# Optimization experiments

Hardware: AMD Instinct MI355X
Metric: run time of the kernel (lower is better)

## Reference

```python
import jax, jax.numpy as jnp
import numpy as np

B, S, FEAT, DK = 128, 2048, 512, 64

def setup_inputs() -> dict:
    key = jax.random.key(0)
    k1, k2, k3, k4, k5 = jax.random.split(key, 5)
    input_k = jax.random.normal(k1, (B, S, FEAT), dtype=jnp.float32)
    input_q = jax.random.normal(k2, (B, FEAT), dtype=jnp.float32)
    context_len = jax.random.randint(k3, (B,), 0, S + 1, dtype=jnp.int32)
    # Linear weights stored as [in, out] so y = x @ W
    W_K = jax.random.normal(k4, (FEAT, DK), dtype=jnp.float32) / np.sqrt(FEAT)
    W_Q = jax.random.normal(k5, (FEAT, DK), dtype=jnp.float32) / np.sqrt(FEAT)
    return {"input_k": input_k, "input_q": input_q, "context_len": context_len,
            "W_K": W_K, "W_Q": W_Q}

def reference(input_k, input_q, context_len, W_K, W_Q):
    # K: [B,S,dk], q: [B,dk]
    K = jnp.einsum('bsf,fd->bsd', input_k, W_K)
    q = input_q @ W_Q
    scores = jnp.einsum('bd,bsd->bs', q, K)  # [B,S] (n_heads=1, no scaling in original)
    mask = jnp.arange(S)[None, :] < context_len[:, None]  # [B,S]
    attn = jax.nn.softmax(jnp.where(mask, scores, -1e30), axis=-1)  # [B,S]
    context = jnp.einsum('bs,bsf->bf', attn, input_k)  # [B,FEAT]
    # length==0 rows produce zeros in the original
    context = jnp.where((context_len > 0)[:, None], context, 0.0)
    return context
```

## Files before the change

### kernel.cpp

```cpp
#include <hip/hip_runtime.h>
#include <math.h>

#define B_    128
#define S_    2048
#define FEAT_ 512
#define DK_   64
#define NSPLIT 32
#define RSTRIDE (NSPLIT * FEAT_)

typedef float f32x4 __attribute__((ext_vector_type(4)));

__device__ __forceinline__ float dot8(f32x4 x0, f32x4 x1, f32x4 v0, f32x4 v1) {
  float p = x0[0] * v0[0];
  p = fmaf(x0[1], v0[1], p);
  p = fmaf(x0[2], v0[2], p);
  p = fmaf(x0[3], v0[3], p);
  p = fmaf(x1[0], v1[0], p);
  p = fmaf(x1[1], v1[1], p);
  p = fmaf(x1[2], v1[2], p);
  p = fmaf(x1[3], v1[3], p);
  return p;
}

__device__ __forceinline__ float wredsum(float p) {
#pragma unroll
  for (int off = 32; off; off >>= 1) p += __shfl_xor(p, off, 64);
  return p;
}

__global__ __launch_bounds__(256) void qv_kernel(
    const float* __restrict__ input_q, const float* __restrict__ W_Q,
    const float* __restrict__ W_K, float* __restrict__ v) {
  int b = blockIdx.x;
  int tid = threadIdx.x;
  __shared__ float xq[FEAT_];
  __shared__ float part[4][DK_];
  __shared__ float qs[DK_];
  for (int f = tid; f < FEAT_; f += 256) xq[f] = input_q[b * FEAT_ + f];
  __syncthreads();
  {
    int d = tid & 63, c = tid >> 6;
    float s = 0.f;
    int f0 = c * 128;
    for (int f = f0; f < f0 + 128; ++f) s = fmaf(xq[f], W_Q[f * DK_ + d], s);
    part[c][d] = s;
  }
  __syncthreads();
  if (tid < DK_)
    qs[tid] = part[0][tid] + part[1][tid] + part[2][tid] + part[3][tid];
  __syncthreads();
  for (int f = tid; f < FEAT_; f += 256) {
    const f32x4* wk = (const f32x4*)(W_K + f * DK_);
    float s = 0.f;
#pragma unroll
    for (int d4 = 0; d4 < DK_ / 4; ++d4) {
      f32x4 w = wk[d4];
      s = fmaf(w[0], qs[d4 * 4 + 0], s);
      s = fmaf(w[1], qs[d4 * 4 + 1], s);
      s = fmaf(w[2], qs[d4 * 4 + 2], s);
      s = fmaf(w[3], qs[d4 * 4 + 3], s);
    }
    v[b * FEAT_ + f] = s;
  }
}

__global__ __launch_bounds__(256) void pass_kernel(
    const float* __restrict__ input_k, const int* __restrict__ ctx,
    const float* __restrict__ v, float* __restrict__ pm,
    float* __restrict__ pl, float* __restrict__ pacc) {
  int split = blockIdx.x;
  int b = blockIdx.y;
  int L = ctx[b];
  int tid = threadIdx.x, wave = tid >> 6, lane = tid & 63;
  int idx = b * NSPLIT + split;

  if (split >= L) {
    if (tid == 0) { pm[idx] = -INFINITY; pl[idx] = 0.f; }
    return;
  }
  int nt = (L - split + NSPLIT - 1) / NSPLIT;

  const float* vb = v + b * FEAT_ + lane * 4;
  f32x4 v0 = *(const f32x4*)vb;
  f32x4 v1 = *(const f32x4*)(vb + 256);

  float m = -INFINITY, l = 0.f;
  f32x4 a0 = {0.f, 0.f, 0.f, 0.f};
  f32x4 a1 = {0.f, 0.f, 0.f, 0.f};

  const float* base = input_k + (size_t)b * S_ * FEAT_ + split * FEAT_ + lane * 4;

  int t = wave;
  for (; t + 12 < nt; t += 16) {
    const float* r_ = base + (size_t)t * RSTRIDE;
    f32x4 x0 = *(const f32x4*)(r_);
    f32x4 x1 = *(const f32x4*)(r_ + 256);
    f32x4 x2 = *(const f32x4*)(r_ + 4 * (size_t)RSTRIDE);
    f32x4 x3 = *(const f32x4*)(r_ + 4 * (size_t)RSTRIDE + 256);
    f32x4 x4 = *(const f32x4*)(r_ + 8 * (size_t)RSTRIDE);
    f32x4 x5 = *(const f32x4*)(r_ + 8 * (size_t)RSTRIDE + 256);
    f32x4 x6 = *(const f32x4*)(r_ + 12 * (size_t)RSTRIDE);
    f32x4 x7 = *(const f32x4*)(r_ + 12 * (size_t)RSTRIDE + 256);

    float p0 = dot8(x0, x1, v0, v1);
    float p1 = dot8(x2, x3, v0, v1);
    float p2 = dot8(x4, x5, v0, v1);
    float p3 = dot8(x6, x7, v0, v1);
    p0 = wredsum(p0);
    p1 = wredsum(p1);
    p2 = wredsum(p2);
    p3 = wredsum(p3);
    float mn = fmaxf(fmaxf(fmaxf(p0, p1), fmaxf(p2, p3)), m);
    float sc = __expf(m - mn);
    float w0 = __expf(p0 - mn), w1 = __expf(p1 - mn);
    float w2 = __expf(p2 - mn), w3 = __expf(p3 - mn);
    l = fmaf(l, sc, (w0 + w1) + (w2 + w3));
#pragma unroll
    for (int j = 0; j < 4; ++j) {
      a0[j] = fmaf(w0, x0[j],
              fmaf(w1, x2[j], fmaf(w2, x4[j], fmaf(w3, x6[j], a0[j] * sc))));
      a1[j] = fmaf(w0, x1[j],
              fmaf(w1, x3[j], fmaf(w2, x5[j], fmaf(w3, x7[j], a1[j] * sc))));
    }
    m = mn;
  }
  for (; t < nt; t += 4) {
    const float* r_ = base + (size_t)t * RSTRIDE;
    f32x4 x0 = *(const f32x4*)(r_);
    f32x4 x1 = *(const f32x4*)(r_ + 256);
    float p = wredsum(dot8(x0, x1, v0, v1));
    float mn = fmaxf(m, p);
    float sc = __expf(m - mn);
    float w = __expf(p - mn);
    l = fmaf(l, sc, w);
#pragma unroll
    for (int j = 0; j < 4; ++j) {
      a0[j] = fmaf(w, x0[j], a0[j] * sc);
      a1[j] = fmaf(w, x1[j], a1[j] * sc);
    }
    m = mn;
  }

  __shared__ float sm[4], sl[4];
  __shared__ float sa[4][FEAT_];
  if (lane == 0) { sm[wave] = m; sl[wave] = l; }
  *(f32x4*)&sa[wave][lane * 4] = a0;
  *(f32x4*)&sa[wave][256 + lane * 4] = a1;
  __syncthreads();

  float M = fmaxf(fmaxf(sm[0], sm[1]), fmaxf(sm[2], sm[3]));
  float e0 = __expf(sm[0] - M), e1 = __expf(sm[1] - M);
  float e2 = __expf(sm[2] - M), e3 = __expf(sm[3] - M);
  if (tid == 0) {
    pm[idx] = M;
    pl[idx] = e0 * sl[0] + e1 * sl[1] + e2 * sl[2] + e3 * sl[3];
  }
  for (int f = tid; f < FEAT_; f += 256)
    pacc[(size_t)idx * FEAT_ + f] =
        e0 * sa[0][f] + e1 * sa[1][f] + e2 * sa[2][f] + e3 * sa[3][f];
}

__global__ __launch_bounds__(256) void combine_kernel(
    const float* __restrict__ pm, const float* __restrict__ pl,
    const float* __restrict__ pacc, float* __restrict__ out) {
  int b = blockIdx.x;
  int tid = threadIdx.x;
  __shared__ float e[NSPLIT];
  __shared__ float inv_s;
  if (tid < NSPLIT) {
    float mi = pm[b * NSPLIT + tid];
    float M = mi;
#pragma unroll
    for (int off = 16; off; off >>= 1) M = fmaxf(M, __shfl_xor(M, off, 64));
    float ei = (M == -INFINITY) ? 0.f : __expf(mi - M);
    e[tid] = ei;
    float lw = ei * pl[b * NSPLIT + tid];
#pragma unroll
    for (int off = 16; off; off >>= 1) lw += __shfl_xor(lw, off, 64);
    if (tid == 0) inv_s = (lw > 0.f) ? 1.f / lw : 0.f;
  }
  __syncthreads();
  float inv = inv_s;
  for (int f = tid; f < FEAT_; f += 256) {
    float s = 0.f;
    for (int i = 0; i < NSPLIT; ++i)
      if (e[i] > 0.f)
        s = fmaf(e[i], pacc[((size_t)(b * NSPLIT + i)) * FEAT_ + f], s);
    out[b * FEAT_ + f] = s * inv;
  }
}

extern "C" void kernel_launch(void* const* d_in, const int* in_sizes, int n_in,
                              void* d_out, int out_size, void* d_ws, size_t ws_size,
                              hipStream_t stream) {
  const float* input_k = (const float*)d_in[0];
  const float* input_q = (const float*)d_in[1];
  const int*   ctx     = (const int*)d_in[2];
  const float* W_K     = (const float*)d_in[3];
  const float* W_Q     = (const float*)d_in[4];
  float* out = (float*)d_out;

  char* ws = (char*)d_ws;
  float* v    = (float*)ws;
  float* pm   = (float*)(ws + (size_t)B_ * FEAT_ * sizeof(float));
  float* pl   = pm + B_ * NSPLIT;
  float* pacc = pl + B_ * NSPLIT;

  qv_kernel<<<B_, 256, 0, stream>>>(input_q, W_Q, W_K, v);
  pass_kernel<<<dim3(NSPLIT, B_), 256, 0, stream>>>(input_k, ctx, v, pm, pl, pacc);
  combine_kernel<<<B_, 256, 0, stream>>>(pm, pl, pacc, out);
}
```

Measured before the change: 78.05 us.

## Split sequence into contiguous chunks per block and halve split count

Each pass block now handles a contiguous range of rows [split*L/NSPLIT, (split+1)*L/NSPLIT) instead of rows strided by NSPLIT, and the split count drops from 32 to 16. Contiguous rows should give better DRAM page and prefetch locality and balance work evenly across splits. Halving the splits also shrinks the partial accumulator traffic and the combine work. The cost is fewer blocks (2048 instead of 4096), which may reduce latency hiding when context lengths are short.

```diff
diff --git a/kernel.cpp b/kernel.cpp
--- a/kernel.cpp
+++ b/kernel.cpp
@@ -5,8 +5,7 @@
 #define S_    2048
 #define FEAT_ 512
 #define DK_   64
-#define NSPLIT 32
-#define RSTRIDE (NSPLIT * FEAT_)
+#define NSPLIT 16
 
 typedef float f32x4 __attribute__((ext_vector_type(4)));
 
@@ -74,11 +73,13 @@
   int tid = threadIdx.x, wave = tid >> 6, lane = tid & 63;
   int idx = b * NSPLIT + split;
 
-  if (split >= L) {
+  int s0 = (split * L) / NSPLIT;
+  int s1 = ((split + 1) * L) / NSPLIT;
+
+  if (s0 >= s1) {
     if (tid == 0) { pm[idx] = -INFINITY; pl[idx] = 0.f; }
     return;
   }
-  int nt = (L - split + NSPLIT - 1) / NSPLIT;
 
   const float* vb = v + b * FEAT_ + lane * 4;
   f32x4 v0 = *(const f32x4*)vb;
@@ -88,19 +89,19 @@
   f32x4 a0 = {0.f, 0.f, 0.f, 0.f};
   f32x4 a1 = {0.f, 0.f, 0.f, 0.f};
 
-  const float* base = input_k + (size_t)b * S_ * FEAT_ + split * FEAT_ + lane * 4;
-
-  int t = wave;
-  for (; t + 12 < nt; t += 16) {
-    const float* r_ = base + (size_t)t * RSTRIDE;
+  const float* base = input_k + (size_t)b * S_ * FEAT_;
+  int s = s0 + wave;
+
+  for (; s + 12 < s1; s += 16) {
+    const float* r_ = base + (size_t)s * FEAT_ + lane * 4;
     f32x4 x0 = *(const f32x4*)(r_);
     f32x4 x1 = *(const f32x4*)(r_ + 256);
-    f32x4 x2 = *(const f32x4*)(r_ + 4 * (size_t)RSTRIDE);
-    f32x4 x3 = *(const f32x4*)(r_ + 4 * (size_t)RSTRIDE + 256);
-    f32x4 x4 = *(const f32x4*)(r_ + 8 * (size_t)RSTRIDE);
-    f32x4 x5 = *(const f32x4*)(r_ + 8 * (size_t)RSTRIDE + 256);
-    f32x4 x6 = *(const f32x4*)(r_ + 12 * (size_t)RSTRIDE);
-    f32x4 x7 = *(const f32x4*)(r_ + 12 * (size_t)RSTRIDE + 256);
+    f32x4 x2 = *(const f32x4*)(r_ + 4 * FEAT_);
+    f32x4 x3 = *(const f32x4*)(r_ + 4 * FEAT_ + 256);
+    f32x4 x4 = *(const f32x4*)(r_ + 8 * FEAT_);
+    f32x4 x5 = *(const f32x4*)(r_ + 8 * FEAT_ + 256);
+    f32x4 x6 = *(const f32x4*)(r_ + 12 * FEAT_);
+    f32x4 x7 = *(const f32x4*)(r_ + 12 * FEAT_ + 256);
 
     float p0 = dot8(x0, x1, v0, v1);
     float p1 = dot8(x2, x3, v0, v1);
@@ -124,8 +125,8 @@
     }
     m = mn;
   }
-  for (; t < nt; t += 4) {
-    const float* r_ = base + (size_t)t * RSTRIDE;
+  for (; s < s1; s += 4) {
+    const float* r_ = base + (size_t)s * FEAT_ + lane * 4;
     f32x4 x0 = *(const f32x4*)(r_);
     f32x4 x1 = *(const f32x4*)(r_ + 256);
     float p = wredsum(dot8(x0, x1, v0, v1));
@@ -171,12 +172,12 @@
     float mi = pm[b * NSPLIT + tid];
     float M = mi;
 #pragma unroll
-    for (int off = 16; off; off >>= 1) M = fmaxf(M, __shfl_xor(M, off, 64));
+    for (int off = 8; off; off >>= 1) M = fmaxf(M, __shfl_xor(M, off, 64));
     float ei = (M == -INFINITY) ? 0.f : __expf(mi - M);
     e[tid] = ei;
     float lw = ei * pl[b * NSPLIT + tid];
 #pragma unroll
-    for (int off = 16; off; off >>= 1) lw += __shfl_xor(lw, off, 64);
+    for (int off = 8; off; off >>= 1) lw += __shfl_xor(lw, off, 64);
     if (tid == 0) inv_s = (lw > 0.f) ? 1.f / lw : 0.f;
   }
   __syncthreads();
```

Measured after the change: 67.19 us. 1.16x faster.
